# Optimization experiments

Hardware: AMD Instinct MI355X
Metric: run time of the kernel (lower is better)

The kernel has to match this reference:

```python
import jax, jax.numpy as jnp
import numpy as np

N_NODES = 100_000
N_EDGES = 1_600_000
IN_CH, HID, OUT_CH = 2, 64, 16


def setup_inputs() -> dict:
    key = jax.random.key(0)
    ks = jax.random.split(key, 6)
    x = jax.random.normal(ks[0], (N_NODES, IN_CH), dtype=jnp.float32)
    edge_index = jax.random.randint(ks[1], (2, N_EDGES), 0, N_NODES, dtype=jnp.int64)
    # Glorot-style init for GCN weights
    W1 = jax.random.normal(ks[2], (IN_CH, HID), dtype=jnp.float32) / np.sqrt(IN_CH)
    b1 = jnp.zeros((HID,), dtype=jnp.float32)
    W_mu = jax.random.normal(ks[3], (HID, OUT_CH), dtype=jnp.float32) / np.sqrt(HID)
    b_mu = jnp.zeros((OUT_CH,), dtype=jnp.float32)
    W_logstd = jax.random.normal(ks[4], (HID, OUT_CH), dtype=jnp.float32) / np.sqrt(HID)
    b_logstd = jnp.zeros((OUT_CH,), dtype=jnp.float32)
    return dict(x=x, edge_index=edge_index, W1=W1, b1=b1,
                W_mu=W_mu, b_mu=b_mu, W_logstd=W_logstd, b_logstd=b_logstd)


def _gcn_conv(x, W, b, src, dst, deg_inv_sqrt, n):
    h = x @ W                                   # [n, out]
    norm = deg_inv_sqrt[src] * deg_inv_sqrt[dst]  # [E]
    agg = jax.ops.segment_sum(norm[:, None] * h[src], dst, num_segments=n)
    agg = agg + (deg_inv_sqrt * deg_inv_sqrt)[:, None] * h  # self-loop term
    return agg + b


def reference(x, edge_index, W1, b1, W_mu, b_mu, W_logstd, b_logstd):
    n = x.shape[0]
    src, dst = edge_index[0], edge_index[1]
    # degree on A+I (self-loop contributes 1)
    deg = 1.0 + jax.ops.segment_sum(jnp.ones_like(src, dtype=x.dtype), dst, num_segments=n)
    dis = jax.lax.rsqrt(deg)
    h = jax.nn.relu(_gcn_conv(x, W1, b1, src, dst, dis, n))
    mu = _gcn_conv(h, W_mu, b_mu, src, dst, dis, n)
    logstd = _gcn_conv(h, W_logstd, b_logstd, src, dst, dis, n)
    return (mu, logstd)
```

## Files before the change

kernel.cpp:

```cpp
#include <hip/hip_runtime.h>
#include <hip/hip_fp16.h>
#include <math.h>


#define CH    4096
#define CAPB  4800

typedef float f32x4 __attribute__((ext_vector_type(4)));

__device__ __forceinline__ float2 cvt2(unsigned u) {
    __half2 h = *reinterpret_cast<__half2*>(&u);
    return __half22float2(h);
}

__device__ __forceinline__ int block_scan512(int* arr, int* tmp, int tid) {
    int v0 = arr[2 * tid], v1 = arr[2 * tid + 1];
    tmp[tid] = v0 + v1;
    __syncthreads();
    for (int off = 1; off < 256; off <<= 1) {
        int a = (tid >= off) ? tmp[tid - off] : 0;
        __syncthreads();
        tmp[tid] += a;
        __syncthreads();
    }
    int incl = tmp[tid];
    int base = incl - v0 - v1;
    arr[2 * tid] = base;
    arr[2 * tid + 1] = base + v0;
    int total = tmp[255];
    __syncthreads();
    return total;
}

__global__ void k_chunksort(const int* __restrict__ src, const int* __restrict__ dst,
                            unsigned* __restrict__ pairsc, unsigned* __restrict__ seg_t,
                            int E, int NC, int NBk) {
    __shared__ int hist[512];
    __shared__ int tmp[256];
    __shared__ int cur[392];
    __shared__ unsigned ebuf[CH];
    int c = blockIdx.x, tid = threadIdx.x;
    int e0 = c * CH;
    int n_e = min(CH, E - e0);

    hist[tid] = 0; hist[tid + 256] = 0;
    __syncthreads();
    for (int i = tid; i < n_e; i += 256) {
        int d = dst[e0 + i];
        atomicAdd(&hist[d >> 8], 1);
    }
    __syncthreads();
    int total = block_scan512(hist, tmp, tid);
    cur[tid] = hist[tid];
    if (tid < 136) cur[tid + 256] = hist[tid + 256];
    __syncthreads();
    for (int i = tid; i < n_e; i += 256) {
        int d = dst[e0 + i];
        int s = src[e0 + i];
        int slot = atomicAdd(&cur[d >> 8], 1);
        ebuf[slot] = ((unsigned)(d & 255) << 17) | (unsigned)s;
    }
    __syncthreads();
    for (int i = tid; i < n_e; i += 256)
        pairsc[(size_t)e0 + i] = ebuf[i];
    for (int b = tid; b < NBk; b += 256) {
        int base = hist[b];
        int next = (b + 1 < 512) ? hist[b + 1] : total;
        seg_t[(size_t)b * NC + c] = ((unsigned)(next - base) << 13) | (unsigned)base;
    }
}

__global__ void k_bucket256(const unsigned* __restrict__ pairsc,
                            const unsigned* __restrict__ seg_t,
                            const float* __restrict__ x,
                            uint2* __restrict__ rows2, float2* __restrict__ xd,
                            int* __restrict__ sorted_src, int NC, int N) {
    __shared__ int coff[512];
    __shared__ int tmp[256];
    __shared__ int hist[512];
    __shared__ int cur[256];
    __shared__ unsigned segs[392];
    __shared__ unsigned lbuf[CAPB];
    __shared__ unsigned sbuf[CAPB];
    int b = blockIdx.x, tid = threadIdx.x;

    for (int c = tid; c < NC; c += 256) segs[c] = seg_t[(size_t)b * NC + c];
    coff[tid] = 0; coff[tid + 256] = 0;
    __syncthreads();
    for (int c = tid; c < NC; c += 256) coff[c] = (int)(segs[c] >> 13);
    __syncthreads();
    int tot = block_scan512(coff, tmp, tid);

    for (int c = tid; c < NC; c += 256) {
        unsigned sg = segs[c];
        int len = (int)(sg >> 13);
        int base = (int)(sg & 0x1FFFu);
        int doff = coff[c];
        const unsigned* p = pairsc + (size_t)c * CH + base;
        for (int j = 0; j < len; ++j) lbuf[doff + j] = p[j];
    }
    hist[tid] = 0; hist[tid + 256] = 0;
    __syncthreads();
    for (int i = tid; i < tot; i += 256) atomicAdd(&hist[lbuf[i] >> 17], 1);
    __syncthreads();
    int deg = hist[tid];
    block_scan512(hist, tmp, tid);
    int excl = hist[tid];
    int n = (b << 8) + tid;
    int ebase = b * CAPB;
    if (n < N) {
        float di = rsqrtf(1.0f + (float)deg);
        rows2[n] = make_uint2((unsigned)(ebase + excl) | ((unsigned)deg << 21),
                              __float_as_uint(di));
        float2 xv = ((const float2*)x)[n];
        xd[n] = make_float2(di * xv.x, di * xv.y);
    }
    cur[tid] = excl;
    __syncthreads();
    for (int i = tid; i < tot; i += 256) {
        unsigned pr = lbuf[i];
        int slot = atomicAdd(&cur[pr >> 17], 1);
        sbuf[slot] = pr & 0x1FFFFu;
    }
    __syncthreads();
    for (int i = tid; i < tot; i += 256)
        sorted_src[ebase + i] = (int)sbuf[i];
}

__global__ void k_mlp(const float2* __restrict__ xd, const uint2* __restrict__ rows2,
                      const int* __restrict__ sorted_src,
                      const float* __restrict__ W1, const float* __restrict__ b1,
                      const float* __restrict__ W_mu, const float* __restrict__ W_logstd,
                      __half* __restrict__ hml16, int N) {
    __shared__ float W1s[128];
    __shared__ float b1s[64];
    __shared__ float Wcs[64 * 32];
    for (int t = threadIdx.x; t < 128; t += 256) W1s[t] = W1[t];
    for (int t = threadIdx.x; t < 64; t += 256) b1s[t] = b1[t];
    for (int t = threadIdx.x; t < 2048; t += 256) {
        int k = t >> 5, c = t & 31;
        Wcs[t] = (c < 16) ? W_mu[k * 16 + c] : W_logstd[k * 16 + (c - 16)];
    }
    __syncthreads();
    int node = blockIdx.x * 8 + (threadIdx.x >> 5);
    int c = threadIdx.x & 31;
    if (node >= N) return;
    uint2 r = rows2[node];
    int beg = (int)(r.x & 0x1FFFFFu);
    int end = beg + (int)(r.x >> 21);
    float di = __uint_as_float(r.y);
    float sx = 0.0f, sy = 0.0f;
    for (int e = beg + c; e < end; e += 32) {
        int s = sorted_src[e];
        float2 u = xd[s];
        sx += u.x;
        sy += u.y;
    }
#pragma unroll
    for (int off = 16; off; off >>= 1) {
        sx += __shfl_xor(sx, off, 32);
        sy += __shfl_xor(sy, off, 32);
    }
    float2 xn = xd[node];
    float axx = di * (sx + xn.x);
    float axy = di * (sy + xn.y);
    float h0 = fmaxf(fmaf(axx, W1s[c],      fmaf(axy, W1s[64 + c],  b1s[c])),      0.0f);
    float h1 = fmaxf(fmaf(axx, W1s[32 + c], fmaf(axy, W1s[96 + c],  b1s[32 + c])), 0.0f);
    float acc = 0.0f;
#pragma unroll
    for (int k = 0; k < 32; ++k) {
        float hk = __shfl(h0, k, 32);
        acc = fmaf(hk, Wcs[k * 32 + c], acc);
    }
#pragma unroll
    for (int k = 0; k < 32; ++k) {
        float hk = __shfl(h1, k, 32);
        acc = fmaf(hk, Wcs[(k + 32) * 32 + c], acc);
    }
    hml16[(size_t)node * 32 + c] = __float2half(di * acc);
}

__global__ void k_agg2(const __half* __restrict__ hml16, const uint2* __restrict__ rows2,
                       const int* __restrict__ sorted_src,
                       const float* __restrict__ b_mu, const float* __restrict__ b_logstd,
                       float* __restrict__ out, int N) {
    int t = blockIdx.x * blockDim.x + threadIdx.x;
    int node = t >> 2, q = t & 3;
    if (node >= N) return;
    const uint4* h4 = (const uint4*)hml16;
    uint2 r = rows2[node];
    int beg = (int)(r.x & 0x1FFFFFu);
    int end = beg + (int)(r.x >> 21);
    float di = __uint_as_float(r.y);
    uint4 v = h4[(size_t)node * 4 + q];
    float2 a0 = cvt2(v.x), a1 = cvt2(v.y), a2 = cvt2(v.z), a3 = cvt2(v.w);
    for (int k = beg; k < end; ++k) {
        int s = sorted_src[k];
        uint4 u = h4[(size_t)s * 4 + q];
        float2 t0 = cvt2(u.x), t1 = cvt2(u.y), t2 = cvt2(u.z), t3 = cvt2(u.w);
        a0.x += t0.x; a0.y += t0.y; a1.x += t1.x; a1.y += t1.y;
        a2.x += t2.x; a2.y += t2.y; a3.x += t3.x; a3.y += t3.y;
    }
    const float* bp = (q < 2) ? (b_mu + 8 * q) : (b_logstd + 8 * (q - 2));
    float* op = out + ((q < 2) ? (size_t)0 : (size_t)N * 16)
                    + (size_t)node * 16 + (size_t)(q & 1) * 8;
    f32x4 r0 = { fmaf(di, a0.x, bp[0]), fmaf(di, a0.y, bp[1]),
                 fmaf(di, a1.x, bp[2]), fmaf(di, a1.y, bp[3]) };
    f32x4 r1 = { fmaf(di, a2.x, bp[4]), fmaf(di, a2.y, bp[5]),
                 fmaf(di, a3.x, bp[6]), fmaf(di, a3.y, bp[7]) };
    *(f32x4*)op = r0;
    *(f32x4*)(op + 4) = r1;
}

extern "C" void kernel_launch(void* const* d_in, const int* in_sizes, int n_in,
                              void* d_out, int out_size, void* d_ws, size_t ws_size,
                              hipStream_t stream) {
    const float* x        = (const float*)d_in[0];
    const int*   eidx     = (const int*)d_in[1];
    const float* W1       = (const float*)d_in[2];
    const float* b1       = (const float*)d_in[3];
    const float* W_mu     = (const float*)d_in[4];
    const float* b_mu     = (const float*)d_in[5];
    const float* W_logstd = (const float*)d_in[6];
    const float* b_logstd = (const float*)d_in[7];
    float* out = (float*)d_out;

    const int N = in_sizes[0] / 2;
    const int E = in_sizes[1] / 2;
    const int NC  = (E + CH - 1) / CH;
    const int NBk = (N + 255) >> 8;

    const int* src = eidx;
    const int* dst = eidx + E;

    char* w = (char*)d_ws;
    auto alloc = [&](size_t bytes) -> void* {
        void* p = (void*)w;
        w += (bytes + 255) & ~(size_t)255;
        return p;
    };
    unsigned* pairsc     = (unsigned*)alloc((size_t)NC * CH * 4);
    unsigned* seg_t      = (unsigned*)alloc((size_t)NBk * NC * 4);
    int*      sorted_src = (int*)     alloc((size_t)NBk * CAPB * 4);
    uint2*    rows2      = (uint2*)   alloc((size_t)N * 8);
    float2*   xd         = (float2*)  alloc((size_t)N * 8);
    __half*   hml16      = (__half*)  alloc((size_t)N * 32 * 2);

    k_chunksort<<<NC, 256, 0, stream>>>(src, dst, pairsc, seg_t, E, NC, NBk);
    k_bucket256<<<NBk, 256, 0, stream>>>(pairsc, seg_t, x, rows2, xd,
                                         sorted_src, NC, N);
    k_mlp      <<<(N + 7) / 8, 256, 0, stream>>>(xd, rows2, sorted_src,
                                                 W1, b1, W_mu, W_logstd, hml16, N);
    k_agg2     <<<(4 * N + 255) / 256, 256, 0, stream>>>(hml16, rows2, sorted_src,
                                                         b_mu, b_logstd, out, N);
}
```

Before: 190.4 us.

## Use 16 lanes per node in MLP kernel with interleaved mu/logstd fp16 layout

The fused first-layer aggregation and dense projection kernel now assigns 16 lanes per node instead of 32, so each block covers twice as many nodes. Each lane computes four hidden units and one interleaved (mu, logstd) output pair, reading W1 and b1 from registers and a packed float2 weight table from shared memory. The intermediate is stored as half2 pairs, and the second aggregation kernel is updated to unpack that interleaved layout. This cuts idle lanes on low-degree neighbor gathers and reduces shuffles and shared memory loads per output, at the cost of more registers per lane.

Measured after the change: 171.2 us. -10.1%, faster.

```diff
diff --git a/kernel.cpp b/kernel.cpp
--- a/kernel.cpp
+++ b/kernel.cpp
@@ -131,56 +131,69 @@
                       const int* __restrict__ sorted_src,
                       const float* __restrict__ W1, const float* __restrict__ b1,
                       const float* __restrict__ W_mu, const float* __restrict__ W_logstd,
-                      __half* __restrict__ hml16, int N) {
-    __shared__ float W1s[128];
-    __shared__ float b1s[64];
-    __shared__ float Wcs[64 * 32];
-    for (int t = threadIdx.x; t < 128; t += 256) W1s[t] = W1[t];
-    for (int t = threadIdx.x; t < 64; t += 256) b1s[t] = b1[t];
-    for (int t = threadIdx.x; t < 2048; t += 256) {
-        int k = t >> 5, c = t & 31;
-        Wcs[t] = (c < 16) ? W_mu[k * 16 + c] : W_logstd[k * 16 + (c - 16)];
-    }
-    __syncthreads();
-    int node = blockIdx.x * 8 + (threadIdx.x >> 5);
-    int c = threadIdx.x & 31;
+                      __half2* __restrict__ hml16, int N) {
+    __shared__ float2 Wp[64 * 16];
+    int tid = threadIdx.x;
+    for (int t = tid; t < 1024; t += 256) {
+        int k = t >> 4, c2 = t & 15;
+        Wp[t] = make_float2(W_mu[k * 16 + c2], W_logstd[k * 16 + c2]);
+    }
+    int c2 = tid & 15;
+    float w1a[4], w1b[4], bb[4];
+#pragma unroll
+    for (int j = 0; j < 4; ++j) {
+        w1a[j] = W1[c2 + 16 * j];
+        w1b[j] = W1[64 + c2 + 16 * j];
+        bb[j]  = b1[c2 + 16 * j];
+    }
+    __syncthreads();
+    int node = blockIdx.x * 16 + (tid >> 4);
     if (node >= N) return;
     uint2 r = rows2[node];
     int beg = (int)(r.x & 0x1FFFFFu);
     int end = beg + (int)(r.x >> 21);
     float di = __uint_as_float(r.y);
     float sx = 0.0f, sy = 0.0f;
-    for (int e = beg + c; e < end; e += 32) {
+    for (int e = beg + c2; e < end; e += 16) {
         int s = sorted_src[e];
         float2 u = xd[s];
         sx += u.x;
         sy += u.y;
     }
 #pragma unroll
-    for (int off = 16; off; off >>= 1) {
-        sx += __shfl_xor(sx, off, 32);
-        sy += __shfl_xor(sy, off, 32);
+    for (int off = 8; off; off >>= 1) {
+        sx += __shfl_xor(sx, off, 16);
+        sy += __shfl_xor(sy, off, 16);
     }
     float2 xn = xd[node];
     float axx = di * (sx + xn.x);
     float axy = di * (sy + xn.y);
-    float h0 = fmaxf(fmaf(axx, W1s[c],      fmaf(axy, W1s[64 + c],  b1s[c])),      0.0f);
-    float h1 = fmaxf(fmaf(axx, W1s[32 + c], fmaf(axy, W1s[96 + c],  b1s[32 + c])), 0.0f);
-    float acc = 0.0f;
-#pragma unroll
-    for (int k = 0; k < 32; ++k) {
-        float hk = __shfl(h0, k, 32);
-        acc = fmaf(hk, Wcs[k * 32 + c], acc);
-    }
-#pragma unroll
-    for (int k = 0; k < 32; ++k) {
-        float hk = __shfl(h1, k, 32);
-        acc = fmaf(hk, Wcs[(k + 32) * 32 + c], acc);
-    }
-    hml16[(size_t)node * 32 + c] = __float2half(di * acc);
-}
-
-__global__ void k_agg2(const __half* __restrict__ hml16, const uint2* __restrict__ rows2,
+    float h[4];
+#pragma unroll
+    for (int j = 0; j < 4; ++j)
+        h[j] = fmaxf(fmaf(axx, w1a[j], fmaf(axy, w1b[j], bb[j])), 0.0f);
+    float2 a0 = make_float2(0.f, 0.f), a1 = a0, a2 = a0, a3 = a0;
+#pragma unroll
+    for (int kk = 0; kk < 16; ++kk) {
+        float h0 = __shfl(h[0], kk, 16);
+        float h1 = __shfl(h[1], kk, 16);
+        float h2 = __shfl(h[2], kk, 16);
+        float h3 = __shfl(h[3], kk, 16);
+        float2 w0 = Wp[kk * 16 + c2];
+        float2 w1 = Wp[(16 + kk) * 16 + c2];
+        float2 w2 = Wp[(32 + kk) * 16 + c2];
+        float2 w3 = Wp[(48 + kk) * 16 + c2];
+        a0.x = fmaf(h0, w0.x, a0.x); a0.y = fmaf(h0, w0.y, a0.y);
+        a1.x = fmaf(h1, w1.x, a1.x); a1.y = fmaf(h1, w1.y, a1.y);
+        a2.x = fmaf(h2, w2.x, a2.x); a2.y = fmaf(h2, w2.y, a2.y);
+        a3.x = fmaf(h3, w3.x, a3.x); a3.y = fmaf(h3, w3.y, a3.y);
+    }
+    float mu = di * ((a0.x + a1.x) + (a2.x + a3.x));
+    float ls = di * ((a0.y + a1.y) + (a2.y + a3.y));
+    hml16[(size_t)node * 16 + c2] = __floats2half2_rn(mu, ls);
+}
+
+__global__ void k_agg2(const __half2* __restrict__ hml16, const uint2* __restrict__ rows2,
                        const int* __restrict__ sorted_src,
                        const float* __restrict__ b_mu, const float* __restrict__ b_logstd,
                        float* __restrict__ out, int N) {
@@ -201,15 +214,14 @@
         a0.x += t0.x; a0.y += t0.y; a1.x += t1.x; a1.y += t1.y;
         a2.x += t2.x; a2.y += t2.y; a3.x += t3.x; a3.y += t3.y;
     }
-    const float* bp = (q < 2) ? (b_mu + 8 * q) : (b_logstd + 8 * (q - 2));
-    float* op = out + ((q < 2) ? (size_t)0 : (size_t)N * 16)
-                    + (size_t)node * 16 + (size_t)(q & 1) * 8;
-    f32x4 r0 = { fmaf(di, a0.x, bp[0]), fmaf(di, a0.y, bp[1]),
-                 fmaf(di, a1.x, bp[2]), fmaf(di, a1.y, bp[3]) };
-    f32x4 r1 = { fmaf(di, a2.x, bp[4]), fmaf(di, a2.y, bp[5]),
-                 fmaf(di, a3.x, bp[6]), fmaf(di, a3.y, bp[7]) };
-    *(f32x4*)op = r0;
-    *(f32x4*)(op + 4) = r1;
+    float4 bm = *(const float4*)(b_mu + 4 * q);
+    float4 bl = *(const float4*)(b_logstd + 4 * q);
+    f32x4 mu = { fmaf(di, a0.x, bm.x), fmaf(di, a1.x, bm.y),
+                 fmaf(di, a2.x, bm.z), fmaf(di, a3.x, bm.w) };
+    f32x4 ls = { fmaf(di, a0.y, bl.x), fmaf(di, a1.y, bl.y),
+                 fmaf(di, a2.y, bl.z), fmaf(di, a3.y, bl.w) };
+    *(f32x4*)(out + (size_t)node * 16 + 4 * q) = mu;
+    *(f32x4*)(out + (size_t)(N + node) * 16 + 4 * q) = ls;
 }
 
 extern "C" void kernel_launch(void* const* d_in, const int* in_sizes, int n_in,
@@ -244,13 +256,13 @@
     int*      sorted_src = (int*)     alloc((size_t)NBk * CAPB * 4);
     uint2*    rows2      = (uint2*)   alloc((size_t)N * 8);
     float2*   xd         = (float2*)  alloc((size_t)N * 8);
-    __half*   hml16      = (__half*)  alloc((size_t)N * 32 * 2);
+    __half2*  hml16      = (__half2*) alloc((size_t)N * 16 * 4);
 
     k_chunksort<<<NC, 256, 0, stream>>>(src, dst, pairsc, seg_t, E, NC, NBk);
     k_bucket256<<<NBk, 256, 0, stream>>>(pairsc, seg_t, x, rows2, xd,
                                          sorted_src, NC, N);
-    k_mlp      <<<(N + 7) / 8, 256, 0, stream>>>(xd, rows2, sorted_src,
-                                                 W1, b1, W_mu, W_logstd, hml16, N);
+    k_mlp      <<<(N + 15) / 16, 256, 0, stream>>>(xd, rows2, sorted_src,
+                                                   W1, b1, W_mu, W_logstd, hml16, N);
     k_agg2     <<<(4 * N + 255) / 256, 256, 0, stream>>>(hml16, rows2, sorted_src,
                                                          b_mu, b_logstd, out, N);
 }
```
